# Performance work log

Hardware: AMD Instinct MI355X
Metric: run time of the kernel (lower is better)

Reference implementation:

```python
import jax, jax.numpy as jnp
import numpy as np

D_IN = 1024
D_OUT = 1024
SEQ = 4096


def setup_inputs() -> dict:
    key = jax.random.key(0)
    kx, kq, kk, kv = jax.random.split(key, 4)
    s = 1.0 / np.sqrt(D_IN)
    return {
        "x": jax.random.normal(kx, (SEQ, D_IN), dtype=jnp.float32),
        # torch Linear weights: shape [d_out, d_in], y = x @ W.T
        "Wq": jax.random.uniform(kq, (D_OUT, D_IN), jnp.float32, -s, s),
        "Wk": jax.random.uniform(kk, (D_OUT, D_IN), jnp.float32, -s, s),
        "Wv": jax.random.uniform(kv, (D_OUT, D_IN), jnp.float32, -s, s),
    }


def reference(x, Wq, Wk, Wv):
    # QKV projections (no bias)
    q = x @ Wq.T  # [N, d_out]
    k = x @ Wk.T
    v = x @ Wv.T
    scale = 1.0 / jnp.sqrt(jnp.asarray(k.shape[-1], x.dtype))
    att = jax.nn.softmax((q @ k.T) * scale, axis=-1)  # [N, N]
    return att @ v  # [N, d_out]
```

## Files before the change

kernel.cpp:

```cpp
#include <hip/hip_runtime.h>
#include <hip/hip_bf16.h>
#include <math.h>

typedef __attribute__((ext_vector_type(8))) short short8;
typedef __attribute__((ext_vector_type(4))) float floatx4;

static __device__ __forceinline__ unsigned short f2bf(float f) {
    union { float f; unsigned int u; } a; a.f = f;
    unsigned int u = a.u;
    return (unsigned short)((u + 0x7FFFu + ((u >> 16) & 1u)) >> 16);
}
static __device__ __forceinline__ float bf2f(unsigned short h) {
    union { unsigned int u; float f; } a; a.u = ((unsigned int)h) << 16;
    return a.f;
}

static __device__ __forceinline__ void cvt8(const float* __restrict__ src,
                                            unsigned short* __restrict__ dst, int i) {
    float4 v0 = *(const float4*)(src + i);
    float4 v1 = *(const float4*)(src + i + 4);
    ushort4 o0, o1;
    o0.x = f2bf(v0.x); o0.y = f2bf(v0.y); o0.z = f2bf(v0.z); o0.w = f2bf(v0.w);
    o1.x = f2bf(v1.x); o1.y = f2bf(v1.y); o1.z = f2bf(v1.z); o1.w = f2bf(v1.w);
    *(ushort4*)(dst + i) = o0;
    *(ushort4*)(dst + i + 4) = o1;
}

struct CV { const float* x; unsigned short* xb;
            const float* W[3]; unsigned short* Wb[3]; float* l; };
__global__ __launch_bounds__(256)
void cvt_all(CV a) {
    int b = blockIdx.x, t = threadIdx.x;
    if (b < 2048) {
        cvt8(a.x, a.xb, (b * 256 + t) * 8);
    } else if (b < 3584) {
        int z  = (b - 2048) >> 9;
        int bb = (b - 2048) & 511;
        cvt8(a.W[z], a.Wb[z], (bb * 256 + t) * 8);
    } else {
        float4 zz = {0.f, 0.f, 0.f, 0.f};
        #pragma unroll
        for (int c = 0; c < 4; c++)
            *(float4*)(a.l + t * 16 + c * 4) = zz;
    }
}

template<int BM, int BN, int BK, int TI, int TJ, int WCOLS>
__device__ __forceinline__ void gemm_core(const unsigned short* __restrict__ A,
                                          const unsigned short* __restrict__ B,
                                          int lda, int k_begin, int k_end,
                                          unsigned short* sA, unsigned short* sB,
                                          floatx4 (&acc)[TI][TJ],
                                          int bm, int bn)
{
    constexpr int CPR = BK / 8;
    constexpr int RPR = 2048 / BK;
    const int t    = threadIdx.x;
    const int wave = t >> 6;
    const int lane = t & 63;
    const int wm = (wave / WCOLS) * (TI * 16);
    const int wn = (wave % WCOLS) * (TJ * 16);

    const int srow   = t / CPR;
    const int schunk = t % CPR;
    const int gchunk = schunk ^ (srow & (CPR - 1));
    const int lm  = lane & 15;
    const int swz = lm & (CPR - 1);

    for (int k0 = k_begin; k0 < k_end; k0 += BK) {
        __syncthreads();
        #pragma unroll
        for (int r = 0; r < (BM * BK) / 2048; r++) {
            const unsigned short* gA =
                A + (size_t)(bm + srow + r * RPR) * lda + k0 + gchunk * 8;
            __builtin_amdgcn_global_load_lds(
                (const __attribute__((address_space(1))) void*)gA,
                (__attribute__((address_space(3))) void*)((char*)sA + wave * 1024 + r * 4096),
                16, 0, 0);
        }
        #pragma unroll
        for (int r = 0; r < (BN * BK) / 2048; r++) {
            const unsigned short* gB =
                B + (size_t)(bn + srow + r * RPR) * lda + k0 + gchunk * 8;
            __builtin_amdgcn_global_load_lds(
                (const __attribute__((address_space(1))) void*)gB,
                (__attribute__((address_space(3))) void*)((char*)sB + wave * 1024 + r * 4096),
                16, 0, 0);
        }
        __syncthreads();

        #pragma unroll
        for (int kk = 0; kk < BK; kk += 32) {
            const int c  = (kk >> 3) + (lane >> 4);
            const int ce = ((c ^ swz) << 3);
            short8 a_frag[TI], b_frag[TJ];
            #pragma unroll
            for (int i = 0; i < TI; i++)
                a_frag[i] = *(const short8*)&sA[(wm + i * 16 + lm) * BK + ce];
            #pragma unroll
            for (int j = 0; j < TJ; j++)
                b_frag[j] = *(const short8*)&sB[(wn + j * 16 + lm) * BK + ce];
            #pragma unroll
            for (int i = 0; i < TI; i++)
                #pragma unroll
                for (int j = 0; j < TJ; j++)
                    acc[i][j] = __builtin_amdgcn_mfma_f32_16x16x32_bf16(
                        a_frag[i], b_frag[j], acc[i][j], 0, 0, 0);
        }
    }
}


struct P3 { const unsigned short* W[3]; unsigned short* O[3]; };
__global__ __launch_bounds__(256)
void proj3(const unsigned short* __restrict__ xb, P3 a) {
    __shared__ unsigned short sA[128 * 128];
    __shared__ unsigned short sB[128 * 128];

    const int lid = blockIdx.x;
    const int xcd = lid & 7;
    const int rem = lid >> 3;
    const int row = (rem & 7) * 4 + (xcd >> 1);
    const int col = ((rem >> 3) & 3) * 2 + (xcd & 1);
    const int z   = rem >> 5;

    const unsigned short* B = a.W[z];
    unsigned short* O = a.O[z];
    const bool trans = (z == 2);
    const float scale = (z == 0) ? 0.03125f : 1.0f;

    floatx4 acc[4][4];
    #pragma unroll
    for (int i = 0; i < 4; i++)
        #pragma unroll
        for (int j = 0; j < 4; j++) { floatx4 zz = {0.f,0.f,0.f,0.f}; acc[i][j] = zz; }

    const int bm = row * 128, bn = col * 128;
    gemm_core<128, 128, 128, 4, 4, 2>(xb, B, 1024, 0, 1024, sA, sB, acc, bm, bn);

    const int lane = threadIdx.x & 63, wave = threadIdx.x >> 6;
    const int wm = (wave >> 1) * 64, wn = (wave & 1) * 64;
    const int lm = lane & 15, rq = (lane >> 4) * 4;
    #pragma unroll
    for (int i = 0; i < 4; i++)
        #pragma unroll
        for (int j = 0; j < 4; j++) {
            int tm = bm + wm + i * 16 + rq;
            int tn = bn + wn + j * 16 + lm;
            if (trans) {
                ushort4 h4;
                h4.x = f2bf(acc[i][j][0]);
                h4.y = f2bf(acc[i][j][1]);
                h4.z = f2bf(acc[i][j][2]);
                h4.w = f2bf(acc[i][j][3]);
                *(ushort4*)&O[(size_t)tn * 4096 + tm] = h4;
            } else {
                #pragma unroll
                for (int r = 0; r < 4; r++)
                    O[(size_t)(tm + r) * 1024 + tn] = f2bf(acc[i][j][r] * scale);
            }
        }
}

__global__ __launch_bounds__(256)
void gemm_ps(const unsigned short* __restrict__ q, const unsigned short* __restrict__ k,
             unsigned short* __restrict__ Pm, float* __restrict__ l) {
    __shared__ unsigned short sA[128 * 128];
    __shared__ unsigned short sB[128 * 128];

    const int lid = blockIdx.x;
    const int xcd = lid & 7;
    const int i8  = lid >> 3;
    const int by  = (xcd & 1) * 16 + (i8 & 15);
    const int bx  = (xcd >> 1) * 8 + (i8 >> 4);

    floatx4 acc[4][4];
    #pragma unroll
    for (int i = 0; i < 4; i++)
        #pragma unroll
        for (int j = 0; j < 4; j++) { floatx4 zz = {0.f,0.f,0.f,0.f}; acc[i][j] = zz; }

    const int bm = by * 128, bn = bx * 128;
    gemm_core<128, 128, 128, 4, 4, 2>(q, k, 1024, 0, 1024, sA, sB, acc, bm, bn);

    const int lane = threadIdx.x & 63, wave = threadIdx.x >> 6;
    const int wm = (wave >> 1) * 64, wn = (wave & 1) * 64;
    const int lm = lane & 15, rq = (lane >> 4) * 4;
    #pragma unroll
    for (int i = 0; i < 4; i++) {
        #pragma unroll
        for (int r = 0; r < 4; r++) {
            int row = bm + wm + i * 16 + rq + r;
            float rs = 0.f;
            #pragma unroll
            for (int j = 0; j < 4; j++) {
                float e = __expf(acc[i][j][r]);
                rs += e;
                int tn = bn + wn + j * 16 + lm;
                Pm[(size_t)row * 4096 + tn] = f2bf(e);
            }
            rs += __shfl_xor(rs, 1);
            rs += __shfl_xor(rs, 2);
            rs += __shfl_xor(rs, 4);
            rs += __shfl_xor(rs, 8);
            if (lm == 0) atomicAdd(l + row, rs);
        }
    }
}

__global__ __launch_bounds__(256)
void gemm_osplit(const unsigned short* __restrict__ Pm, const unsigned short* __restrict__ vT,
                 unsigned short* __restrict__ Opart) {
    __shared__ unsigned short sA[128 * 128];
    __shared__ unsigned short sB[128 * 128];

    const int lid = blockIdx.x;
    const int xcd = lid & 7;
    const int w   = lid >> 6;
    const int g   = (lid >> 3) & 7;
    const int s   = w * 8 + xcd;
    const int z   = s >> 5;
    const int row = s & 31;

    floatx4 acc[4][4];
    #pragma unroll
    for (int i = 0; i < 4; i++)
        #pragma unroll
        for (int j = 0; j < 4; j++) { floatx4 zz = {0.f,0.f,0.f,0.f}; acc[i][j] = zz; }

    const int bm = row * 128, bn = g * 128;
    gemm_core<128, 128, 128, 4, 4, 2>(Pm, vT, 4096, z * 2048, (z + 1) * 2048,
                                      sA, sB, acc, bm, bn);

    unsigned short* Op = Opart + (size_t)z * (4096 * 1024);
    const int lane = threadIdx.x & 63, wave = threadIdx.x >> 6;
    const int wm = (wave >> 1) * 64, wn = (wave & 1) * 64;
    const int lm = lane & 15, rq = (lane >> 4) * 4;
    #pragma unroll
    for (int i = 0; i < 4; i++)
        #pragma unroll
        for (int j = 0; j < 4; j++) {
            int tm = bm + wm + i * 16 + rq;
            int tn = bn + wn + j * 16 + lm;
            #pragma unroll
            for (int r = 0; r < 4; r++)
                Op[(size_t)(tm + r) * 1024 + tn] = f2bf(acc[i][j][r]);
        }
}

__global__ __launch_bounds__(256)
void reduce_scale(const unsigned short* __restrict__ Op, const float* __restrict__ l,
                  float* __restrict__ out) {
    int i = (blockIdx.x * 256 + threadIdx.x) * 4;
    ushort4 a = *(const ushort4*)(Op + i);
    ushort4 b = *(const ushort4*)(Op + 4096 * 1024 + i);
    float inv = 1.0f / l[i >> 10];
    float4 o;
    o.x = (bf2f(a.x) + bf2f(b.x)) * inv;
    o.y = (bf2f(a.y) + bf2f(b.y)) * inv;
    o.z = (bf2f(a.z) + bf2f(b.z)) * inv;
    o.w = (bf2f(a.w) + bf2f(b.w)) * inv;
    *(float4*)(out + i) = o;
}

extern "C" void kernel_launch(void* const* d_in, const int* in_sizes, int n_in,
                              void* d_out, int out_size, void* d_ws, size_t ws_size,
                              hipStream_t stream) {
    const float* x  = (const float*)d_in[0];
    const float* Wq = (const float*)d_in[1];
    const float* Wk = (const float*)d_in[2];
    const float* Wv = (const float*)d_in[3];
    float* out = (float*)d_out;

    const int SEQ = 4096, D = 1024;
    char* ws = (char*)d_ws;
    const size_t MB = 1u << 20;
    unsigned short* vTb = (unsigned short*)(ws);
    unsigned short* xb  = (unsigned short*)(ws + 8 * MB);
    unsigned short* Wqb = (unsigned short*)(ws + 16 * MB);
    unsigned short* Wkb = (unsigned short*)(ws + 18 * MB);
    unsigned short* Wvb = (unsigned short*)(ws + 20 * MB);
    unsigned short* qb  = (unsigned short*)(ws + 22 * MB);
    unsigned short* kb  = (unsigned short*)(ws + 30 * MB);
    unsigned short* P   = (unsigned short*)(ws + 38 * MB);
    float*          l   = (float*)(ws + 70 * MB);
    unsigned short* Opart = (unsigned short*)(ws + 72 * MB);

    dim3 blk(256);
    CV cv = {x, xb, {Wq, Wk, Wv}, {Wqb, Wkb, Wvb}, l};
    cvt_all<<<dim3(3585), blk, 0, stream>>>(cv);

    P3 p3 = {{Wqb, Wkb, Wvb}, {qb, kb, vTb}};
    proj3<<<dim3(768), blk, 0, stream>>>(xb, p3);

    gemm_ps<<<dim3(1024), blk, 0, stream>>>(qb, kb, P, l);

    gemm_osplit<<<dim3(512), blk, 0, stream>>>(P, vTb, Opart);

    reduce_scale<<<(SEQ * D) / 1024, blk, 0, stream>>>(Opart, l, out);
}
```

Before: 200.3 us.

## Fuse split-K reduction into PV GEMM epilogue via float atomics; shrink QK^T BK

Removes the bf16 partial-output buffer and the separate reduce_scale kernel. The split-K PV GEMM now scales by 1/l and atomically adds fp32 results straight into the output, which the conversion kernel zeroes beforehand. This saves one launch plus a 16MB write and read of partials, in exchange for 4M scattered fp32 atomic adds whose summation order is nondeterministic. The QK^T GEMM also drops its K tile from 128 to 64, halving shared memory, likely to raise occupancy.

Result: slower. 227.1 us (+13.4%).

```diff
diff --git a/kernel.cpp b/kernel.cpp
--- a/kernel.cpp
+++ b/kernel.cpp
@@ -9,10 +9,6 @@
     union { float f; unsigned int u; } a; a.f = f;
     unsigned int u = a.u;
     return (unsigned short)((u + 0x7FFFu + ((u >> 16) & 1u)) >> 16);
-}
-static __device__ __forceinline__ float bf2f(unsigned short h) {
-    union { unsigned int u; float f; } a; a.u = ((unsigned int)h) << 16;
-    return a.f;
 }
 
 static __device__ __forceinline__ void cvt8(const float* __restrict__ src,
@@ -27,7 +23,8 @@
 }
 
 struct CV { const float* x; unsigned short* xb;
-            const float* W[3]; unsigned short* Wb[3]; float* l; };
+            const float* W[3]; unsigned short* Wb[3];
+            float* l; float* out; };
 __global__ __launch_bounds__(256)
 void cvt_all(CV a) {
     int b = blockIdx.x, t = threadIdx.x;
@@ -37,11 +34,14 @@
         int z  = (b - 2048) >> 9;
         int bb = (b - 2048) & 511;
         cvt8(a.W[z], a.Wb[z], (bb * 256 + t) * 8);
+    } else if (b == 3584) {
+        float4 zz = {0.f, 0.f, 0.f, 0.f};
+        #pragma unroll
+        for (int c = 0; c < 4; c++)
+            *(float4*)(a.l + t * 16 + c * 4) = zz;
     } else {
         float4 zz = {0.f, 0.f, 0.f, 0.f};
-        #pragma unroll
-        for (int c = 0; c < 4; c++)
-            *(float4*)(a.l + t * 16 + c * 4) = zz;
+        *(float4*)(a.out + ((b - 3585) * 256 + t) * 4) = zz;
     }
 }
 
@@ -165,8 +165,8 @@
 __global__ __launch_bounds__(256)
 void gemm_ps(const unsigned short* __restrict__ q, const unsigned short* __restrict__ k,
              unsigned short* __restrict__ Pm, float* __restrict__ l) {
-    __shared__ unsigned short sA[128 * 128];
-    __shared__ unsigned short sB[128 * 128];
+    __shared__ unsigned short sA[128 * 64];
+    __shared__ unsigned short sB[128 * 64];
 
     const int lid = blockIdx.x;
     const int xcd = lid & 7;
@@ -181,7 +181,7 @@
         for (int j = 0; j < 4; j++) { floatx4 zz = {0.f,0.f,0.f,0.f}; acc[i][j] = zz; }
 
     const int bm = by * 128, bn = bx * 128;
-    gemm_core<128, 128, 128, 4, 4, 2>(q, k, 1024, 0, 1024, sA, sB, acc, bm, bn);
+    gemm_core<128, 128, 64, 4, 4, 2>(q, k, 1024, 0, 1024, sA, sB, acc, bm, bn);
 
     const int lane = threadIdx.x & 63, wave = threadIdx.x >> 6;
     const int wm = (wave >> 1) * 64, wn = (wave & 1) * 64;
@@ -210,7 +210,7 @@
 
 __global__ __launch_bounds__(256)
 void gemm_osplit(const unsigned short* __restrict__ Pm, const unsigned short* __restrict__ vT,
-                 unsigned short* __restrict__ Opart) {
+                 const float* __restrict__ l, float* __restrict__ out) {
     __shared__ unsigned short sA[128 * 128];
     __shared__ unsigned short sB[128 * 128];
 
@@ -232,35 +232,23 @@
     gemm_core<128, 128, 128, 4, 4, 2>(Pm, vT, 4096, z * 2048, (z + 1) * 2048,
                                       sA, sB, acc, bm, bn);
 
-    unsigned short* Op = Opart + (size_t)z * (4096 * 1024);
     const int lane = threadIdx.x & 63, wave = threadIdx.x >> 6;
     const int wm = (wave >> 1) * 64, wn = (wave & 1) * 64;
     const int lm = lane & 15, rq = (lane >> 4) * 4;
     #pragma unroll
-    for (int i = 0; i < 4; i++)
+    for (int i = 0; i < 4; i++) {
+        int tm = bm + wm + i * 16 + rq;
+        float inv[4];
+        #pragma unroll
+        for (int r = 0; r < 4; r++) inv[r] = 1.0f / l[tm + r];
         #pragma unroll
         for (int j = 0; j < 4; j++) {
-            int tm = bm + wm + i * 16 + rq;
             int tn = bn + wn + j * 16 + lm;
             #pragma unroll
             for (int r = 0; r < 4; r++)
-                Op[(size_t)(tm + r) * 1024 + tn] = f2bf(acc[i][j][r]);
-        }
-}
-
-__global__ __launch_bounds__(256)
-void reduce_scale(const unsigned short* __restrict__ Op, const float* __restrict__ l,
-                  float* __restrict__ out) {
-    int i = (blockIdx.x * 256 + threadIdx.x) * 4;
-    ushort4 a = *(const ushort4*)(Op + i);
-    ushort4 b = *(const ushort4*)(Op + 4096 * 1024 + i);
-    float inv = 1.0f / l[i >> 10];
-    float4 o;
-    o.x = (bf2f(a.x) + bf2f(b.x)) * inv;
-    o.y = (bf2f(a.y) + bf2f(b.y)) * inv;
-    o.z = (bf2f(a.z) + bf2f(b.z)) * inv;
-    o.w = (bf2f(a.w) + bf2f(b.w)) * inv;
-    *(float4*)(out + i) = o;
+                atomicAdd(&out[(size_t)(tm + r) * 1024 + tn], acc[i][j][r] * inv[r]);
+        }
+    }
 }
 
 extern "C" void kernel_launch(void* const* d_in, const int* in_sizes, int n_in,
@@ -284,18 +272,15 @@
     unsigned short* kb  = (unsigned short*)(ws + 30 * MB);
     unsigned short* P   = (unsigned short*)(ws + 38 * MB);
     float*          l   = (float*)(ws + 70 * MB);
-    unsigned short* Opart = (unsigned short*)(ws + 72 * MB);
 
     dim3 blk(256);
-    CV cv = {x, xb, {Wq, Wk, Wv}, {Wqb, Wkb, Wvb}, l};
-    cvt_all<<<dim3(3585), blk, 0, stream>>>(cv);
+    CV cv = {x, xb, {Wq, Wk, Wv}, {Wqb, Wkb, Wvb}, l, out};
+    cvt_all<<<dim3(7681), blk, 0, stream>>>(cv);
 
     P3 p3 = {{Wqb, Wkb, Wvb}, {qb, kb, vTb}};
     proj3<<<dim3(768), blk, 0, stream>>>(xb, p3);
 
     gemm_ps<<<dim3(1024), blk, 0, stream>>>(qb, kb, P, l);
 
-    gemm_osplit<<<dim3(512), blk, 0, stream>>>(P, vTb, Opart);
-
-    reduce_scale<<<(SEQ * D) / 1024, blk, 0, stream>>>(Opart, l, out);
-}
+    gemm_osplit<<<dim3(512), blk, 0, stream>>>(P, vTb, l, out);
+}
```
